# Kernel tuning notes

Measured on AMD Instinct MI355X. Metric: run time of the kernel, lower is better.

Reference implementation:

```python
import jax, jax.numpy as jnp
import numpy as np
from jax import lax

BS, TLEN, N, S = 256, 3, 90, 65
CHEV, TF, NC = 45, 10, 2
FEAT = (N - 2) * (CHEV - 2)          # 88*43 = 3784
FLAT = TLEN * FEAT                    # 11352
BN_EPS = 1e-5
DN = ('NCHW', 'OIHW', 'NCHW')


def _pearson_cheb_adj(x):
    """x: (B, N, S) -> (B, 3, N, N): [T0=I, T1=L_tilde, T2=2*L*T1-T0 (elementwise)]."""
    xc = x - x.mean(axis=2, keepdims=True)
    y = xc / (jnp.linalg.norm(xc, axis=2, keepdims=True) + 1e-6)
    corr = jnp.einsum('bns,bms->bnm', y, y)
    W = (corr + 1.0) * 0.5
    I = jnp.eye(N, dtype=W.dtype)
    L = I[None] * jnp.sum(W, axis=2)[:, :, None] - W          # D - W, symmetric PSD
    # original uses torch.linalg.eig + .item() (detached); eigvalsh is equivalent for symmetric L
    lam = lax.stop_gradient(jnp.max(jnp.abs(jnp.linalg.eigvalsh(L)), axis=1))
    Lt = 2.0 * L / lam[:, None, None] - I
    T0 = jnp.broadcast_to(I, Lt.shape)
    T2 = 2.0 * Lt * Lt - T0                                   # elementwise, per cheb_polynomial
    return jnp.stack([T0, Lt, T2], axis=1)


def _bn_eval(x, g, b):
    # eval-mode BatchNorm1d with running_mean=0, running_var=1
    return x * (g / jnp.sqrt(jnp.float32(1.0 + BN_EPS))) + b


def setup_inputs() -> dict:
    key = jax.random.key(0)
    ks = jax.random.split(key, 12)
    rn = lambda k, shp, s: jax.random.normal(k, shp, dtype=jnp.float32) * s
    return {
        'fdata':   rn(ks[0], (BS, TLEN, N, S), 1.0),
        'un_w':    rn(ks[1], (N * S, 1), 0.01),
        'un_b':    jnp.zeros((1,), jnp.float32),
        'theta':   rn(ks[2], (3, S, CHEV), 0.05),
        'tconv_w': rn(ks[3], (TF, TLEN, 3, 3), 0.1),
        'tconv_b': jnp.zeros((TF,), jnp.float32),
        'oconv_w': rn(ks[4], (1, TF, 1, 1), 0.1),
        'oconv_b': jnp.zeros((1,), jnp.float32),
        'l1_w':    rn(ks[5], (FLAT, 1024), 0.01),
        'l1_b':    jnp.zeros((1024,), jnp.float32),
        'bn1_g':   jnp.ones((1024,), jnp.float32),
        'bn1_b':   jnp.zeros((1024,), jnp.float32),
        'l2_w':    rn(ks[6], (1024, 256), 0.03),
        'l2_b':    jnp.zeros((256,), jnp.float32),
        'bn2_g':   jnp.ones((256,), jnp.float32),
        'bn2_b':   jnp.zeros((256,), jnp.float32),
        'l3_w':    rn(ks[7], (256, NC), 0.06),
        'l3_b':    jnp.zeros((NC,), jnp.float32),
    }


def reference(fdata, un_w, un_b, theta, tconv_w, tconv_b, oconv_w, oconv_b,
              l1_w, l1_b, bn1_g, bn1_b, l2_w, l2_b, bn2_g, bn2_b, l3_w, l3_b):
    bs, tlen, n, s = fdata.shape
    fp = jnp.transpose(fdata, (1, 0, 2, 3))                    # (tlen, bs, N, S)

    # Uncertainty head (replicates original's tlen-major reshape then bs-major view)
    u = fp.reshape(tlen * bs, n * s) @ un_w + un_b
    cs = jax.nn.sigmoid(u.reshape(bs, tlen, 1))                # (bs, tlen, 1)

    # per-(sample,timestep) pearson Laplacian + Chebyshev basis
    adj = _pearson_cheb_adj(fp.reshape(tlen * bs, n, s))       # (tlen*bs, 3, N, N)
    adj = adj.reshape(tlen, bs, 3, n, n)

    def st_block(adj_t):                                       # adj_t: (bs, 3, N, N)
        h = jax.nn.relu(jnp.einsum('bknm,btms,kso->btno', adj_t, fdata, theta))  # (bs,tlen,N,45)
        c = lax.conv_general_dilated(h, tconv_w, (1, 1), 'VALID', dimension_numbers=DN)
        c = jax.nn.relu(c + tconv_b[None, :, None, None])      # (bs,10,88,43)
        o = lax.conv_general_dilated(c, oconv_w, (1, 1), 'VALID', dimension_numbers=DN)
        return o + oconv_b[None, :, None, None]                # (bs,1,88,43)

    block = jax.vmap(st_block)(adj)                            # (tlen, bs, 1, 88, 43)
    block = block.squeeze(2).reshape(tlen, bs, -1)             # (tlen, bs, 3784)
    block = jnp.transpose(block, (1, 0, 2))                    # (bs, tlen, 3784)

    # sum_s cs[b,s] * block[b,t,f]  ==  block * cs.sum(axis=1) (original broadcast quirk)
    final = block * jnp.sum(cs, axis=1)[:, :, None]            # (bs, tlen, 3784)

    x = final.reshape(bs, -1)                                  # (bs, 11352)
    x = _bn_eval(x @ l1_w + l1_b, bn1_g, bn1_b)
    x = _bn_eval(x @ l2_w + l2_b, bn2_g, bn2_b)
    return jax.nn.softmax(x @ l3_w + l3_b, axis=1)
```

## Files before the change

kernel.cpp:

```cpp
#include <hip/hip_runtime.h>
#include <math.h>

#define TPB 256

constexpr int BSZ = 256, TL = 3, NV = 90, SV = 65, CH = 45;
constexpr int NS = NV*SV;
constexpr int NP = TL*BSZ;
constexpr int NM = NV*NV;
constexpr int CCOL = TL*CH;
constexpr int ZLD = 136;
constexpr int CONV_H = 88, CONV_W = 43, FEAT = CONV_H*CONV_W;
constexpr int FLATD = TL*FEAT;

constexpr size_t OFF_CSUM = 0;
constexpr size_t OFF_LAM  = 256;
constexpr size_t OFF_BEFF = 1024;
constexpr size_t OFF_M    = 1056;
constexpr size_t OFF_MA   = 3104;
constexpr size_t OFF_WEFF = 5152;
constexpr size_t OFF_L    = 32768;
constexpr size_t OFF_Z    = 6291456;
constexpr size_t OFF_X    = 15728640;

__global__ __launch_bounds__(TPB) void k_prep(const float* __restrict__ fdata,
    const float* __restrict__ unw, const float* __restrict__ unb,
    float* __restrict__ Lout, float* __restrict__ lamOut, float* __restrict__ csum)
{
    __shared__ float yT[65*96];
    __shared__ float Ll[90*92];
    __shared__ float Dl[NV];
    __shared__ float vbuf[2][92];
    __shared__ float red[TPB];
    __shared__ float sh0, sh1;

    const int q = blockIdx.x, tid = threadIdx.x;
    const int t = q >> 8, b = q & 255;
    const float* xp = fdata + ((size_t)b*TL + t)*NS;
    const int wave = tid >> 6, lane = tid & 63;

    float up = 0.f;
    for (int n = wave; n < NV; n += 4) {
        const float* row = xp + n*SV;
        float va = row[lane];
        float vb = (lane == 0) ? row[64] : 0.f;
        up += va*unw[n*SV + lane];
        if (lane == 0) up += vb*unw[n*SV + 64];
        float s1 = va + vb, s2 = va*va + vb*vb;
        #pragma unroll
        for (int o = 1; o < 64; o <<= 1) { s1 += __shfl_xor(s1, o); s2 += __shfl_xor(s2, o); }
        float mean = s1 / SV;
        float var  = s2 - SV*mean*mean;
        float inv  = 1.f / (sqrtf(fmaxf(var, 0.f)) + 1e-6f);
        yT[lane*96 + (((n >> 2) + lane) % 24)*4 + (n & 3)] = (va - mean)*inv;
        if (lane == 0)
            yT[64*96 + (((n >> 2) + 64) % 24)*4 + (n & 3)] = (vb - mean)*inv;
    }
    red[tid] = up; __syncthreads();
    if (tid < 128) red[tid] += red[tid+128]; __syncthreads();
    if (tid < 64)  red[tid] += red[tid+64];  __syncthreads();
    if (tid < 64) {
        float x = red[tid];
        #pragma unroll
        for (int o = 32; o >= 1; o >>= 1) x += __shfl_down(x, o);
        if (tid == 0) {
            float u = x + unb[0];
            atomicAdd(csum + (q/3), 1.f/(1.f + expf(-u)));
        }
    }
    __syncthreads();

    for (int tile = tid; tile < 529; tile += TPB) {
        int tr = tile / 23, tc = tile - tr*23;
        int n0 = 4*tr, m0 = 4*tc;
        int ca = tr, cb = tc;
        float acc[4][4] = {};
        for (int s = 0; s < SV; ++s) {
            const float* base = &yT[s*96];
            float4 a4 = *(const float4*)(base + 4*ca);
            float4 b4 = *(const float4*)(base + 4*cb);
            float av[4] = {a4.x, a4.y, a4.z, a4.w};
            float bv[4] = {b4.x, b4.y, b4.z, b4.w};
            #pragma unroll
            for (int i = 0; i < 4; ++i)
                #pragma unroll
                for (int j = 0; j < 4; ++j) acc[i][j] += av[i]*bv[j];
            if (++ca == 24) ca = 0;
            if (++cb == 24) cb = 0;
        }
        #pragma unroll
        for (int i = 0; i < 4; ++i) {
            int n = n0 + i; if (n >= NV) break;
            #pragma unroll
            for (int j = 0; j < 4; ++j) {
                int m = m0 + j;
                if (m < NV) Ll[n*92 + m] = (acc[i][j] + 1.f)*0.5f;
            }
        }
    }
    __syncthreads();

    if (tid < NV) {
        float d = 0.f;
        for (int m = 0; m < NV; ++m) d += Ll[tid*92 + m];
        Dl[tid] = d;
    }
    __syncthreads();

    for (int idx = tid; idx < NM; idx += TPB) {
        int n = idx / NV, m = idx - n*NV;
        float v = ((n == m) ? Dl[n] : 0.f) - Ll[n*92 + m];
        Ll[n*92 + m] = v;
        Lout[(size_t)q*NM + idx] = v;
    }
    __syncthreads();

    float r[90];
    if (tid < NV) {
        const float4* row4 = (const float4*)&Ll[tid*92];
        #pragma unroll
        for (int j = 0; j < 22; ++j) {
            float4 x = row4[j];
            r[4*j] = x.x; r[4*j+1] = x.y; r[4*j+2] = x.z; r[4*j+3] = x.w;
        }
        r[88] = Ll[tid*92 + 88]; r[89] = Ll[tid*92 + 89];
        vbuf[0][tid] = sinf(1.3f*tid + 0.5f) + 0.05f;
    }
    if (tid >= 90 && tid < 92) { vbuf[0][tid] = 0.f; vbuf[1][tid] = 0.f; }
    __syncthreads();

    int cur = 0;
    auto step = [&](float sigma) {
        if (tid < NV) {
            const float4* v4 = (const float4*)&vbuf[cur][0];
            float p = 0.f;
            #pragma unroll
            for (int j = 0; j < 22; ++j) {
                float4 x = v4[j];
                p += r[4*j]*x.x + r[4*j+1]*x.y + r[4*j+2]*x.z + r[4*j+3]*x.w;
            }
            p += r[88]*vbuf[cur][88] + r[89]*vbuf[cur][89];
            vbuf[cur^1][tid] = p - sigma*vbuf[cur][tid];
        }
        __syncthreads();
        cur ^= 1;
    };
    auto renorm = [&]() {
        if (tid < 64) {
            float xa = vbuf[cur][tid], xb = (tid < 26) ? vbuf[cur][64+tid] : 0.f;
            float a1 = xa + xb, a2 = xa*xa + xb*xb;
            #pragma unroll
            for (int o = 1; o < 64; o <<= 1) { a1 += __shfl_xor(a1, o); a2 += __shfl_xor(a2, o); }
            if (tid == 0) { sh0 = a1; sh1 = a2; }
        }
        __syncthreads();
        float mean = sh0*(1.f/90.f);
        float ns   = sh1 - 90.f*mean*mean;
        float rn   = rsqrtf(fmaxf(ns, 1e-30f));
        if (tid < NV) vbuf[cur][tid] = (vbuf[cur][tid] - mean)*rn;
        __syncthreads();
    };
    auto dot_vw = [&]() {
        if (tid < 64) {
            float p = vbuf[cur][tid]*vbuf[cur^1][tid];
            if (tid < 26) p += vbuf[cur][64+tid]*vbuf[cur^1][64+tid];
            #pragma unroll
            for (int o = 1; o < 64; o <<= 1) p += __shfl_xor(p, o);
            if (tid == 0) sh0 = p;
        }
        __syncthreads();
    };

    for (int it = 0; it < 8; ++it) step(0.f);
    renorm();
    step(0.f);
    cur ^= 1;
    dot_vw();
    float sigma = 0.45f*sh0;
    __syncthreads();
    if (tid < NV) vbuf[cur^1][tid] -= sigma*vbuf[cur][tid];
    __syncthreads();
    cur ^= 1;
    for (int it = 0; it < 88; ++it) {
        step(sigma);
        if ((it & 7) == 7) renorm();
    }
    renorm();
    step(0.f);
    cur ^= 1;
    dot_vw();
    if (tid == 0) lamOut[q] = sh0;
}

__global__ __launch_bounds__(TPB) void k_Z(const float* __restrict__ fdata,
                                           const float* __restrict__ theta,
                                           float* __restrict__ Z)
{
    __shared__ float flT[65*96];
    __shared__ float thl[3*65*48];

    const int g = blockIdx.x, tid = threadIdx.x;
    const int b = g/3, tp = g - 3*b;
    const float* fp = fdata + ((size_t)b*TL + tp)*NS;

    for (int idx = tid; idx < 65*96; idx += TPB) {
        int s = idx / 96, m = idx - s*96;
        flT[idx] = (m < NV) ? fp[m*SV + s] : 0.f;
    }
    for (int idx = tid; idx < 3*65*48; idx += TPB) {
        int k = idx / (65*48), rr = idx - k*(65*48);
        int s = rr / 48, o = rr - s*48;
        thl[idx] = (o < CH) ? theta[(k*SV + s)*CH + o] : 0.f;
    }
    __syncthreads();

    for (int tile = tid; tile < 432; tile += TPB) {
        int ct = tile / 12, mt = tile - ct*12;
        int k = ct / 12, ot = ct - k*12;
        int o0 = 4*ot, m0 = 8*mt;
        float acc[8][4] = {};
        const float4* thp = (const float4*)&thl[(k*65)*48 + o0];
        const float4* fp4 = (const float4*)&flT[m0];
        for (int s = 0; s < SV; ++s) {
            float4 tv = thp[s*12];
            float4 fa = fp4[s*24], fb = fp4[s*24 + 1];
            float fv[8] = {fa.x, fa.y, fa.z, fa.w, fb.x, fb.y, fb.z, fb.w};
            #pragma unroll
            for (int i = 0; i < 8; ++i) {
                acc[i][0] += fv[i]*tv.x; acc[i][1] += fv[i]*tv.y;
                acc[i][2] += fv[i]*tv.z; acc[i][3] += fv[i]*tv.w;
            }
        }
        #pragma unroll
        for (int i = 0; i < 8; ++i) {
            int m = m0 + i; if (m >= NV) break;
            #pragma unroll
            for (int j = 0; j < 4; ++j) {
                int o = o0 + j;
                if (o < CH)
                    Z[((size_t)(k*BSZ + b)*NV + m)*ZLD + tp*CH + o] = acc[i][j];
            }
        }
    }
    if (tp == 2) {
        for (int idx = tid; idx < 3*NV; idx += TPB) {
            int k = idx / NV, m = idx - k*NV;
            Z[((size_t)(k*BSZ + b)*NV + m)*ZLD + 135] = 0.f;
        }
    }
}

__global__ __launch_bounds__(TPB) void k_hc(const float* __restrict__ L,
    const float* __restrict__ lam, const float* __restrict__ Z,
    const float* __restrict__ tw, const float* __restrict__ tb,
    const float* __restrict__ ow, const float* __restrict__ ob,
    const float* __restrict__ csum, float* __restrict__ X)
{
    __shared__ float smem[12160];
    const int q = blockIdx.x, tid = threadIdx.x;
    const int t = q >> 8, b = q & 255;
    const float il2 = 2.0f / lam[q];

    for (int idx = tid; idx < NM; idx += TPB) {
        int i = idx / NV, j = idx - i*NV;
        smem[i*92 + j] = il2 * L[(size_t)q*NM + idx] - ((i == j) ? 1.f : 0.f);
    }
    __syncthreads();

    float acc[6][8];
    const int tn = tid / 17, tc = tid - tn*17;
    const int n0 = 6*tn, c0 = 8*tc;
    const bool act = (tid < 255);
    if (act) {
        #pragma unroll
        for (int i = 0; i < 6; ++i)
            #pragma unroll
            for (int j = 0; j < 8; ++j) acc[i][j] = 0.f;
        const float* z1p = Z + ((size_t)(BSZ + b)*NV)*ZLD + c0;
        const float* z2p = Z + ((size_t)(2*BSZ + b)*NV)*ZLD + c0;
        for (int m = 0; m < NV; ++m) {
            const float* ar = &smem[m*92 + n0];
            float2 a01 = *(const float2*)(ar);
            float2 a23 = *(const float2*)(ar + 2);
            float2 a45 = *(const float2*)(ar + 4);
            float av[6] = {a01.x, a01.y, a23.x, a23.y, a45.x, a45.y};
            const float4* z1r = (const float4*)(z1p + (size_t)m*ZLD);
            const float4* z2r = (const float4*)(z2p + (size_t)m*ZLD);
            float4 z1a = z1r[0], z1b = z1r[1];
            float4 z2a = z2r[0], z2b = z2r[1];
            float zv1[8] = {z1a.x,z1a.y,z1a.z,z1a.w,z1b.x,z1b.y,z1b.z,z1b.w};
            float zv2[8] = {z2a.x,z2a.y,z2a.z,z2a.w,z2b.x,z2b.y,z2b.z,z2b.w};
            #pragma unroll
            for (int i = 0; i < 6; ++i) {
                float a = av[i], bb = 2.f*a*a;
                #pragma unroll
                for (int j = 0; j < 8; ++j) acc[i][j] += a*zv1[j] + bb*zv2[j];
            }
        }
    }
    __syncthreads();

    float (*hl)[NV][CH] = (float (*)[NV][CH])smem;
    if (act) {
        const float* z0p = Z + ((size_t)b*NV)*ZLD;
        const float* z2p = Z + ((size_t)(2*BSZ + b)*NV)*ZLD;
        #pragma unroll
        for (int i = 0; i < 6; ++i) {
            int n = n0 + i;
            const float4* z0r = (const float4*)(z0p + (size_t)n*ZLD + c0);
            const float4* z2r = (const float4*)(z2p + (size_t)n*ZLD + c0);
            float4 z0a = z0r[0], z0b = z0r[1];
            float4 w2a = z2r[0], w2b = z2r[1];
            float zv0[8] = {z0a.x,z0a.y,z0a.z,z0a.w,z0b.x,z0b.y,z0b.z,z0b.w};
            float zv2[8] = {w2a.x,w2a.y,w2a.z,w2a.w,w2b.x,w2b.y,w2b.z,w2b.w};
            #pragma unroll
            for (int j = 0; j < 8; ++j) {
                int c = c0 + j;
                if (c < CCOL) {
                    float v = fmaxf(acc[i][j] + zv0[j] - zv2[j], 0.f);
                    hl[c/CH][n][c - (c/CH)*CH] = v;
                }
            }
        }
    }
    __syncthreads();

    const float cs  = csum[b];
    const float obv = ob[0];
    float* Xo = X + (size_t)b*FLATD + (size_t)t*FEAT;
    for (int g = tid; g < 88*11; g += TPB) {
        int i = g / 11, jg = g - (g/11)*11, j0 = 4*jg;
        float cf[10][4];
        #pragma unroll
        for (int f = 0; f < 10; ++f) {
            float bv = tb[f];
            cf[f][0] = bv; cf[f][1] = bv; cf[f][2] = bv; cf[f][3] = bv;
        }
        #pragma unroll
        for (int tp = 0; tp < 3; ++tp)
            #pragma unroll
            for (int di = 0; di < 3; ++di) {
                const float* hr = &hl[tp][i + di][j0];
                float w0 = hr[0], w1 = hr[1], w2 = hr[2],
                      w3 = hr[3], w4 = hr[4], w5 = hr[5];
                #pragma unroll
                for (int f = 0; f < 10; ++f) {
                    const float* twp = tw + ((f*TL + tp)*3 + di)*3;
                    float t0 = twp[0], t1 = twp[1], t2 = twp[2];
                    cf[f][0] += w0*t0 + w1*t1 + w2*t2;
                    cf[f][1] += w1*t0 + w2*t1 + w3*t2;
                    cf[f][2] += w2*t0 + w3*t1 + w4*t2;
                    cf[f][3] += w3*t0 + w4*t1 + w5*t2;
                }
            }
        float a0 = 0.f, a1 = 0.f, a2 = 0.f, a3 = 0.f;
        #pragma unroll
        for (int f = 0; f < 10; ++f) {
            float o = ow[f];
            a0 += fmaxf(cf[f][0], 0.f)*o; a1 += fmaxf(cf[f][1], 0.f)*o;
            a2 += fmaxf(cf[f][2], 0.f)*o; a3 += fmaxf(cf[f][3], 0.f)*o;
        }
        int pixb = i*CONV_W + j0;
        Xo[pixb] = (a0 + obv)*cs;
        if (j0 + 1 < CONV_W) Xo[pixb+1] = (a1 + obv)*cs;
        if (j0 + 2 < CONV_W) Xo[pixb+2] = (a2 + obv)*cs;
        if (j0 + 3 < CONV_W) Xo[pixb+3] = (a3 + obv)*cs;
    }
}

__global__ void k_eff1(const float* __restrict__ W2, const float* __restrict__ g2,
                       const float* __restrict__ W3, const float* __restrict__ g1,
                       float* __restrict__ M, float* __restrict__ Ma)
{
    int gid = blockIdx.x*TPB + threadIdx.x;
    if (gid >= 2048) return;
    int i = gid >> 1, c = gid & 1;
    const float rs = rsqrtf(1.f + 1e-5f);
    float acc = 0.f;
    for (int j = 0; j < 256; ++j) acc += W2[i*256 + j]*(g2[j]*rs)*W3[j*2 + c];
    M[gid]  = acc;
    Ma[gid] = acc*(g1[i]*rs);
}

__global__ void k_effb(const float* __restrict__ M, const float* __restrict__ W3,
                       const float* __restrict__ b1, const float* __restrict__ bb1, const float* __restrict__ g1,
                       const float* __restrict__ b2, const float* __restrict__ bb2, const float* __restrict__ g2,
                       const float* __restrict__ b3, float* __restrict__ beff)
{
    __shared__ float r0[TPB], r1[TPB];
    int tid = threadIdx.x;
    const float rs = rsqrtf(1.f + 1e-5f);
    float a0 = 0.f, a1 = 0.f;
    for (int i = tid; i < 1024; i += TPB) {
        float wv = b1[i]*(g1[i]*rs) + bb1[i];
        a0 += wv*M[2*i]; a1 += wv*M[2*i+1];
    }
    for (int j = tid; j < 256; j += TPB) {
        float wv = b2[j]*(g2[j]*rs) + bb2[j];
        a0 += wv*W3[2*j]; a1 += wv*W3[2*j+1];
    }
    r0[tid] = a0; r1[tid] = a1; __syncthreads();
    if (tid < 128) { r0[tid] += r0[tid+128]; r1[tid] += r1[tid+128]; } __syncthreads();
    if (tid < 64)  { r0[tid] += r0[tid+64];  r1[tid] += r1[tid+64];  } __syncthreads();
    if (tid < 64) {
        float x0 = r0[tid], x1 = r1[tid];
        #pragma unroll
        for (int o = 32; o >= 1; o >>= 1) { x0 += __shfl_down(x0, o); x1 += __shfl_down(x1, o); }
        if (tid == 0) { beff[0] = x0 + b3[0]; beff[1] = x1 + b3[1]; }
    }
}

__global__ void k_eff2(const float* __restrict__ W1, const float* __restrict__ Ma,
                       float* __restrict__ Weff)
{
    int tid = threadIdx.x;
    int r = blockIdx.x*4 + (tid >> 6);
    int lane = tid & 63;
    if (r >= FLATD) return;
    const float* wrow = W1 + (size_t)r*1024;
    float a0 = 0.f, a1 = 0.f;
    for (int i = lane; i < 1024; i += 64) {
        float w = wrow[i];
        a0 += w*Ma[2*i]; a1 += w*Ma[2*i+1];
    }
    #pragma unroll
    for (int o = 32; o >= 1; o >>= 1) { a0 += __shfl_down(a0, o); a1 += __shfl_down(a1, o); }
    if (lane == 0) { Weff[2*r] = a0; Weff[2*r+1] = a1; }
}

__global__ void k_logits(const float* __restrict__ x, const float* __restrict__ Weff,
                         const float* __restrict__ beff, float* __restrict__ out)
{
    __shared__ float r0[TPB], r1[TPB];
    int b = blockIdx.x, tid = threadIdx.x;
    const float* xr = x + (size_t)b*FLATD;
    float a0 = 0.f, a1 = 0.f;
    for (int i = tid; i < FLATD; i += TPB) {
        float v = xr[i];
        a0 += v*Weff[2*i]; a1 += v*Weff[2*i+1];
    }
    r0[tid] = a0; r1[tid] = a1; __syncthreads();
    if (tid < 128) { r0[tid] += r0[tid+128]; r1[tid] += r1[tid+128]; } __syncthreads();
    if (tid < 64)  { r0[tid] += r0[tid+64];  r1[tid] += r1[tid+64];  } __syncthreads();
    if (tid < 64) {
        float x0 = r0[tid], x1 = r1[tid];
        #pragma unroll
        for (int o = 32; o >= 1; o >>= 1) { x0 += __shfl_down(x0, o); x1 += __shfl_down(x1, o); }
        if (tid == 0) {
            float l0 = x0 + beff[0], l1 = x1 + beff[1];
            float mx = fmaxf(l0, l1);
            float e0 = expf(l0 - mx), e1 = expf(l1 - mx);
            float s = e0 + e1;
            out[2*b]     = e0/s;
            out[2*b + 1] = e1/s;
        }
    }
}

extern "C" void kernel_launch(void* const* d_in, const int* in_sizes, int n_in,
                              void* d_out, int out_size, void* d_ws, size_t ws_size,
                              hipStream_t stream)
{
    const float* fdata = (const float*)d_in[0];
    const float* un_w  = (const float*)d_in[1];
    const float* un_b  = (const float*)d_in[2];
    const float* theta = (const float*)d_in[3];
    const float* tcw   = (const float*)d_in[4];
    const float* tcb   = (const float*)d_in[5];
    const float* ocw   = (const float*)d_in[6];
    const float* ocb   = (const float*)d_in[7];
    const float* l1w   = (const float*)d_in[8];
    const float* l1b   = (const float*)d_in[9];
    const float* bn1g  = (const float*)d_in[10];
    const float* bn1b  = (const float*)d_in[11];
    const float* l2w   = (const float*)d_in[12];
    const float* l2b   = (const float*)d_in[13];
    const float* bn2g  = (const float*)d_in[14];
    const float* bn2b  = (const float*)d_in[15];
    const float* l3w   = (const float*)d_in[16];
    const float* l3b   = (const float*)d_in[17];

    float* ws   = (float*)d_ws;
    float* csum = ws + OFF_CSUM;
    float* lam  = ws + OFF_LAM;
    float* beff = ws + OFF_BEFF;
    float* M    = ws + OFF_M;
    float* Ma   = ws + OFF_MA;
    float* Weff = ws + OFF_WEFF;
    float* L    = ws + OFF_L;
    float* Z    = ws + OFF_Z;
    float* X    = ws + OFF_X;
    float* out  = (float*)d_out;

    hipMemsetAsync(csum, 0, BSZ*sizeof(float), stream);
    k_prep <<<NP, TPB, 0, stream>>>(fdata, un_w, un_b, L, lam, csum);
    k_Z    <<<BSZ*TL, TPB, 0, stream>>>(fdata, theta, Z);
    k_hc   <<<NP, TPB, 0, stream>>>(L, lam, Z, tcw, tcb, ocw, ocb, csum, X);
    k_eff1 <<<8, TPB, 0, stream>>>(l2w, bn2g, l3w, bn1g, M, Ma);
    k_effb <<<1, TPB, 0, stream>>>(M, l3w, l1b, bn1b, bn1g, l2b, bn2b, bn2g, l3b, beff);
    k_eff2 <<<(FLATD + 3)/4, TPB, 0, stream>>>(l1w, Ma, Weff);
    k_logits<<<BSZ, TPB, 0, stream>>>(X, Weff, beff, out);
}
```

Before: 557.9 us.

## Split power iteration into wave-per-matrix eigen kernel and retile Z GEMM

```diff
diff --git a/kernel.cpp b/kernel.cpp
--- a/kernel.cpp
+++ b/kernel.cpp
@@ -22,21 +22,20 @@
 constexpr size_t OFF_Z    = 6291456;
 constexpr size_t OFF_X    = 15728640;
 
-__global__ __launch_bounds__(TPB) void k_prep(const float* __restrict__ fdata,
+__global__ __launch_bounds__(TPB) void k_corr(const float* __restrict__ fdata,
     const float* __restrict__ unw, const float* __restrict__ unb,
-    float* __restrict__ Lout, float* __restrict__ lamOut, float* __restrict__ csum)
+    float* __restrict__ Lout, float* __restrict__ csum)
 {
     __shared__ float yT[65*96];
-    __shared__ float Ll[90*92];
-    __shared__ float Dl[NV];
-    __shared__ float vbuf[2][92];
+    __shared__ float Dl[NV], Wd[NV];
     __shared__ float red[TPB];
-    __shared__ float sh0, sh1;
 
     const int q = blockIdx.x, tid = threadIdx.x;
     const int t = q >> 8, b = q & 255;
     const float* xp = fdata + ((size_t)b*TL + t)*NS;
     const int wave = tid >> 6, lane = tid & 63;
+
+    if (tid < NV) Dl[tid] = 0.f;
 
     float up = 0.f;
     for (int n = wave; n < NV; n += 4) {
@@ -69,6 +68,7 @@
     }
     __syncthreads();
 
+    float* Lq = Lout + (size_t)q*NM;
     for (int tile = tid; tile < 529; tile += TPB) {
         int tr = tile / 23, tc = tile - tr*23;
         int n0 = 4*tr, m0 = 4*tc;
@@ -89,155 +89,156 @@
         }
         #pragma unroll
         for (int i = 0; i < 4; ++i) {
-            int n = n0 + i; if (n >= NV) break;
+            int n = n0 + i;
+            if (n >= NV) break;
+            float rsum = 0.f;
             #pragma unroll
             for (int j = 0; j < 4; ++j) {
                 int m = m0 + j;
-                if (m < NV) Ll[n*92 + m] = (acc[i][j] + 1.f)*0.5f;
+                if (m < NV) {
+                    float w = (acc[i][j] + 1.f)*0.5f;
+                    rsum += w;
+                    if (n != m) Lq[n*NV + m] = -w;
+                    else        Wd[n] = w;
+                }
             }
+            atomicAdd(&Dl[n], rsum);
         }
     }
     __syncthreads();
-
-    if (tid < NV) {
-        float d = 0.f;
-        for (int m = 0; m < NV; ++m) d += Ll[tid*92 + m];
-        Dl[tid] = d;
-    }
-    __syncthreads();
-
-    for (int idx = tid; idx < NM; idx += TPB) {
-        int n = idx / NV, m = idx - n*NV;
-        float v = ((n == m) ? Dl[n] : 0.f) - Ll[n*92 + m];
-        Ll[n*92 + m] = v;
-        Lout[(size_t)q*NM + idx] = v;
-    }
-    __syncthreads();
-
-    float r[90];
-    if (tid < NV) {
-        const float4* row4 = (const float4*)&Ll[tid*92];
-        #pragma unroll
-        for (int j = 0; j < 22; ++j) {
-            float4 x = row4[j];
-            r[4*j] = x.x; r[4*j+1] = x.y; r[4*j+2] = x.z; r[4*j+3] = x.w;
-        }
-        r[88] = Ll[tid*92 + 88]; r[89] = Ll[tid*92 + 89];
-        vbuf[0][tid] = sinf(1.3f*tid + 0.5f) + 0.05f;
-    }
-    if (tid >= 90 && tid < 92) { vbuf[0][tid] = 0.f; vbuf[1][tid] = 0.f; }
-    __syncthreads();
-
+    if (tid < NV) Lq[tid*(NV+1)] = Dl[tid] - Wd[tid];
+}
+
+__global__ __launch_bounds__(TPB) void k_eig(const float* __restrict__ L,
+                                             float* __restrict__ lamOut)
+{
+    __shared__ float vbuf[4][2][92];
+    const int tid = threadIdx.x, w = tid >> 6, lane = tid & 63;
+    const int q = blockIdx.x*4 + w;
+    const float* Lq = L + (size_t)q*NM;
+
+    float LA[92], LB[92];
+    {
+        const float2* ra = (const float2*)(Lq + lane*NV);
+        #pragma unroll
+        for (int j = 0; j < 45; ++j) { float2 x = ra[j]; LA[2*j] = x.x; LA[2*j+1] = x.y; }
+        LA[90] = 0.f; LA[91] = 0.f;
+        if (lane < 26) {
+            const float2* rb = (const float2*)(Lq + (64 + lane)*NV);
+            #pragma unroll
+            for (int j = 0; j < 45; ++j) { float2 x = rb[j]; LB[2*j] = x.x; LB[2*j+1] = x.y; }
+        } else {
+            #pragma unroll
+            for (int j = 0; j < 90; ++j) LB[j] = 0.f;
+        }
+        LB[90] = 0.f; LB[91] = 0.f;
+    }
+    if (lane < 2) { vbuf[w][0][90+lane] = 0.f; vbuf[w][1][90+lane] = 0.f; }
+
+    float vA = sinf(1.3f*lane + 0.5f) + 0.05f;
+    float vB = (lane < 26) ? (sinf(1.3f*(64 + lane) + 0.5f) + 0.05f) : 0.f;
     int cur = 0;
-    auto step = [&](float sigma) {
-        if (tid < NV) {
-            const float4* v4 = (const float4*)&vbuf[cur][0];
-            float p = 0.f;
-            #pragma unroll
-            for (int j = 0; j < 22; ++j) {
-                float4 x = v4[j];
-                p += r[4*j]*x.x + r[4*j+1]*x.y + r[4*j+2]*x.z + r[4*j+3]*x.w;
-            }
-            p += r[88]*vbuf[cur][88] + r[89]*vbuf[cur][89];
-            vbuf[cur^1][tid] = p - sigma*vbuf[cur][tid];
-        }
+    float wA = 0.f, wB = 0.f;
+
+    auto share = [&]() {
+        vbuf[w][cur][lane] = vA;
+        if (lane < 26) vbuf[w][cur][64 + lane] = vB;
         __syncthreads();
+    };
+    auto matvec = [&](float sigma) {
+        const float4* v4 = (const float4*)&vbuf[w][cur][0];
+        float p0=0.f,p1=0.f,p2=0.f,p3=0.f, r0=0.f,r1=0.f,r2=0.f,r3=0.f;
+        #pragma unroll
+        for (int j = 0; j < 23; ++j) {
+            float4 x = v4[j];
+            p0 += LA[4*j]*x.x;   p1 += LA[4*j+1]*x.y;
+            p2 += LA[4*j+2]*x.z; p3 += LA[4*j+3]*x.w;
+            r0 += LB[4*j]*x.x;   r1 += LB[4*j+1]*x.y;
+            r2 += LB[4*j+2]*x.z; r3 += LB[4*j+3]*x.w;
+        }
+        wA = (p0+p1) + (p2+p3) - sigma*vA;
+        wB = (r0+r1) + (r2+r3) - sigma*vB;
         cur ^= 1;
     };
     auto renorm = [&]() {
-        if (tid < 64) {
-            float xa = vbuf[cur][tid], xb = (tid < 26) ? vbuf[cur][64+tid] : 0.f;
-            float a1 = xa + xb, a2 = xa*xa + xb*xb;
-            #pragma unroll
-            for (int o = 1; o < 64; o <<= 1) { a1 += __shfl_xor(a1, o); a2 += __shfl_xor(a2, o); }
-            if (tid == 0) { sh0 = a1; sh1 = a2; }
-        }
-        __syncthreads();
-        float mean = sh0*(1.f/90.f);
-        float ns   = sh1 - 90.f*mean*mean;
+        float t1 = vA + ((lane < 26) ? vB : 0.f);
+        float t2 = vA*vA + ((lane < 26) ? vB*vB : 0.f);
+        #pragma unroll
+        for (int o = 1; o < 64; o <<= 1) { t1 += __shfl_xor(t1, o); t2 += __shfl_xor(t2, o); }
+        float mean = t1*(1.f/90.f);
+        float ns   = t2 - 90.f*mean*mean;
         float rn   = rsqrtf(fmaxf(ns, 1e-30f));
-        if (tid < NV) vbuf[cur][tid] = (vbuf[cur][tid] - mean)*rn;
-        __syncthreads();
+        vA = (vA - mean)*rn; vB = (vB - mean)*rn;
     };
-    auto dot_vw = [&]() {
-        if (tid < 64) {
-            float p = vbuf[cur][tid]*vbuf[cur^1][tid];
-            if (tid < 26) p += vbuf[cur][64+tid]*vbuf[cur^1][64+tid];
-            #pragma unroll
-            for (int o = 1; o < 64; o <<= 1) p += __shfl_xor(p, o);
-            if (tid == 0) sh0 = p;
-        }
-        __syncthreads();
+    auto dotvw = [&]() {
+        float d = vA*wA + ((lane < 26) ? vB*wB : 0.f);
+        #pragma unroll
+        for (int o = 1; o < 64; o <<= 1) d += __shfl_xor(d, o);
+        return d;
     };
 
-    for (int it = 0; it < 8; ++it) step(0.f);
+    for (int it = 0; it < 8; ++it) { share(); matvec(0.f); vA = wA; vB = wB; }
     renorm();
-    step(0.f);
-    cur ^= 1;
-    dot_vw();
-    float sigma = 0.45f*sh0;
-    __syncthreads();
-    if (tid < NV) vbuf[cur^1][tid] -= sigma*vbuf[cur][tid];
-    __syncthreads();
-    cur ^= 1;
-    for (int it = 0; it < 88; ++it) {
-        step(sigma);
+    share(); matvec(0.f);
+    float ray = dotvw();
+    float sigma = 0.45f*ray;
+    vA = wA - sigma*vA; vB = wB - sigma*vB;
+    for (int it = 0; it < 87; ++it) {
         if ((it & 7) == 7) renorm();
+        share(); matvec(sigma); vA = wA; vB = wB;
     }
     renorm();
-    step(0.f);
-    cur ^= 1;
-    dot_vw();
-    if (tid == 0) lamOut[q] = sh0;
+    share(); matvec(0.f);
+    float lam = dotvw();
+    if (lane == 0) lamOut[q] = lam;
 }
 
 __global__ __launch_bounds__(TPB) void k_Z(const float* __restrict__ fdata,
                                            const float* __restrict__ theta,
                                            float* __restrict__ Z)
 {
-    __shared__ float flT[65*96];
-    __shared__ float thl[3*65*48];
+    __shared__ float fl[NV][69];
+    __shared__ float thl[3][SV][48];
 
     const int g = blockIdx.x, tid = threadIdx.x;
     const int b = g/3, tp = g - 3*b;
     const float* fp = fdata + ((size_t)b*TL + tp)*NS;
 
-    for (int idx = tid; idx < 65*96; idx += TPB) {
-        int s = idx / 96, m = idx - s*96;
-        flT[idx] = (m < NV) ? fp[m*SV + s] : 0.f;
-    }
-    for (int idx = tid; idx < 3*65*48; idx += TPB) {
-        int k = idx / (65*48), rr = idx - k*(65*48);
+    for (int idx = tid; idx < NS; idx += TPB) {
+        int m = idx / SV, s = idx - m*SV;
+        fl[m][s] = fp[idx];
+    }
+    for (int idx = tid; idx < 3*SV*48; idx += TPB) {
+        int k = idx / (SV*48), rr = idx - k*(SV*48);
         int s = rr / 48, o = rr - s*48;
-        thl[idx] = (o < CH) ? theta[(k*SV + s)*CH + o] : 0.f;
+        thl[k][s][o] = (o < CH) ? theta[(k*SV + s)*CH + o] : 0.f;
     }
     __syncthreads();
 
-    for (int tile = tid; tile < 432; tile += TPB) {
-        int ct = tile / 12, mt = tile - ct*12;
-        int k = ct / 12, ot = ct - k*12;
-        int o0 = 4*ot, m0 = 8*mt;
-        float acc[8][4] = {};
-        const float4* thp = (const float4*)&thl[(k*65)*48 + o0];
-        const float4* fp4 = (const float4*)&flT[m0];
+    for (int tile = tid; tile < 414; tile += TPB) {
+        int mt = tile / 18, ct = tile - mt*18;
+        int k = ct / 6, ot = ct - 6*k;
+        int m0 = 4*mt, o0 = 8*ot;
+        float acc[4][8] = {};
         for (int s = 0; s < SV; ++s) {
-            float4 tv = thp[s*12];
-            float4 fa = fp4[s*24], fb = fp4[s*24 + 1];
-            float fv[8] = {fa.x, fa.y, fa.z, fa.w, fb.x, fb.y, fb.z, fb.w};
-            #pragma unroll
-            for (int i = 0; i < 8; ++i) {
-                acc[i][0] += fv[i]*tv.x; acc[i][1] += fv[i]*tv.y;
-                acc[i][2] += fv[i]*tv.z; acc[i][3] += fv[i]*tv.w;
+            float a0 = fl[m0][s], a1 = fl[m0+1][s], a2 = fl[m0+2][s], a3 = fl[m0+3][s];
+            float4 t0 = *(const float4*)&thl[k][s][o0];
+            float4 t1 = *(const float4*)&thl[k][s][o0+4];
+            float tv[8] = {t0.x,t0.y,t0.z,t0.w,t1.x,t1.y,t1.z,t1.w};
+            #pragma unroll
+            for (int j = 0; j < 8; ++j) {
+                acc[0][j] += a0*tv[j]; acc[1][j] += a1*tv[j];
+                acc[2][j] += a2*tv[j]; acc[3][j] += a3*tv[j];
             }
         }
         #pragma unroll
-        for (int i = 0; i < 8; ++i) {
+        for (int i = 0; i < 4; ++i) {
             int m = m0 + i; if (m >= NV) break;
-            #pragma unroll
-            for (int j = 0; j < 4; ++j) {
+            float* zp = Z + ((size_t)(k*BSZ + b)*NV + m)*ZLD + tp*CH;
+            #pragma unroll
+            for (int j = 0; j < 8; ++j) {
                 int o = o0 + j;
-                if (o < CH)
-                    Z[((size_t)(k*BSZ + b)*NV + m)*ZLD + tp*CH + o] = acc[i][j];
+                if (o < CH) zp[o] = acc[i][j];
             }
         }
     }
@@ -492,7 +493,8 @@
     float* out  = (float*)d_out;
 
     hipMemsetAsync(csum, 0, BSZ*sizeof(float), stream);
-    k_prep <<<NP, TPB, 0, stream>>>(fdata, un_w, un_b, L, lam, csum);
+    k_corr <<<NP, TPB, 0, stream>>>(fdata, un_w, un_b, L, csum);
+    k_eig  <<<NP/4, TPB, 0, stream>>>(L, lam);
     k_Z    <<<BSZ*TL, TPB, 0, stream>>>(fdata, theta, Z);
     k_hc   <<<NP, TPB, 0, stream>>>(L, lam, Z, tcw, tcb, ocw, ocb, csum, X);
     k_eff1 <<<8, TPB, 0, stream>>>(l2w, bn2g, l3w, bn1g, M, Ma);
```

New measurement: 512.5 us. 8.1% less time.
